# Kernel tuning notes

Hardware: AMD Instinct MI355X
Metric: run time of the kernel (lower is better)

Reference implementation:

```python
import jax, jax.numpy as jnp
import numpy as np

N, E = 50000, 800000
IN_DIM, HID, HEADS, OUT_DIM, EDGE_DIM = 128, 32, 4, 64, 32


def _glorot(key, shape, dtype=jnp.float32):
    fan_in, fan_out = shape[0], shape[1]
    lim = np.sqrt(6.0 / (fan_in + fan_out))
    return jax.random.uniform(key, shape, dtype, -lim, lim)


def setup_inputs() -> dict:
    key = jax.random.key(0)
    ks = jax.random.split(key, 16)
    H1 = HEADS * HID  # 128 = concat width of layer 1
    inp = {
        "x": jax.random.normal(ks[0], (N, IN_DIM), jnp.float32),
        "edge_index": jax.random.randint(ks[1], (2, E), 0, N, jnp.int64),
        "edge_feats": jax.random.normal(ks[2], (E, EDGE_DIM), jnp.float32),
        # layer 1: TransformerConv(128 -> 32, heads=4, concat=True, edge_dim=32)
        "Wq1": _glorot(ks[3], (IN_DIM, H1)), "bq1": jnp.zeros((H1,), jnp.float32),
        "Wk1": _glorot(ks[4], (IN_DIM, H1)), "bk1": jnp.zeros((H1,), jnp.float32),
        "Wv1": _glorot(ks[5], (IN_DIM, H1)), "bv1": jnp.zeros((H1,), jnp.float32),
        "We1": _glorot(ks[6], (EDGE_DIM, H1)),
        "Ws1": _glorot(ks[7], (IN_DIM, H1)), "bs1": jnp.zeros((H1,), jnp.float32),
        # layer 2: TransformerConv(128 -> 64, heads=1, concat=False, edge_dim=32)
        "Wq2": _glorot(ks[8], (H1, OUT_DIM)), "bq2": jnp.zeros((OUT_DIM,), jnp.float32),
        "Wk2": _glorot(ks[9], (H1, OUT_DIM)), "bk2": jnp.zeros((OUT_DIM,), jnp.float32),
        "Wv2": _glorot(ks[10], (H1, OUT_DIM)), "bv2": jnp.zeros((OUT_DIM,), jnp.float32),
        "We2": _glorot(ks[11], (EDGE_DIM, OUT_DIM)),
        "Ws2": _glorot(ks[12], (H1, OUT_DIM)), "bs2": jnp.zeros((OUT_DIM,), jnp.float32),
    }
    return inp


def _tconv(x, src, dst, e, Wq, bq, Wk, bk, Wv, bv, We, Ws, bs, heads, concat):
    """PyG TransformerConv: gather q_i/k_j/v_j, add edge embedding to k and v,
    segment-softmax over incoming edges of each target node, scatter-aggregate."""
    n = x.shape[0]
    d = Wq.shape[1] // heads
    q = (x @ Wq + bq).reshape(n, heads, d)
    k = (x @ Wk + bk).reshape(n, heads, d)
    v = (x @ Wv + bv).reshape(n, heads, d)
    ee = (e @ We).reshape(-1, heads, d)      # [E, H, D]
    kj = k[src] + ee                          # [E, H, D]
    vj = v[src] + ee                          # [E, H, D]
    a = jnp.einsum('ehd,ehd->eh', q[dst], kj) / jnp.sqrt(jnp.asarray(d, x.dtype))
    amax = jax.ops.segment_max(a, dst, num_segments=n)      # [N, H]
    ex = jnp.exp(a - amax[dst])
    den = jax.ops.segment_sum(ex, dst, num_segments=n)
    alpha = ex / den[dst]                                   # [E, H]
    out = jax.ops.segment_sum(alpha[..., None] * vj, dst, num_segments=n)
    out = out.reshape(n, heads * d) if concat else out.mean(axis=1)
    return out + x @ Ws + bs  # root/skip connection (lin_skip)


def reference(x, edge_index, edge_feats,
              Wq1, bq1, Wk1, bk1, Wv1, bv1, We1, Ws1, bs1,
              Wq2, bq2, Wk2, bk2, Wv2, bv2, We2, Ws2, bs2):
    src, dst = edge_index[0], edge_index[1]  # flow='source_to_target'
    h = _tconv(x, src, dst, edge_feats, Wq1, bq1, Wk1, bk1, Wv1, bv1,
               We1, Ws1, bs1, heads=HEADS, concat=True)
    h = jax.nn.relu(h)  # activation; dropout p=0.0 is identity
    h = _tconv(h, src, dst, edge_feats, Wq2, bq2, Wk2, bk2, Wv2, bv2,
               We2, Ws2, bs2, heads=1, concat=False)
    return h
```

## Files before the change

kernel.cpp:

```cpp
#include <hip/hip_runtime.h>
#include <hip/hip_bf16.h>


typedef unsigned int  u32;
typedef unsigned short u16;
typedef __attribute__((ext_vector_type(8))) __bf16 bf16x8;
typedef __attribute__((ext_vector_type(4))) float  f32x4;

#define S1L (0.17677669529663687f * 1.4426950408889634f)
#define S2L (0.125f * 1.4426950408889634f)

__device__ __forceinline__ u16 f2bf(float f) {
    u32 u = __float_as_uint(f);
    u32 r = (u + 0x7fffu + ((u >> 16) & 1u)) >> 16;
    return (u16)r;
}
__device__ __forceinline__ float bflo(u32 u) { return __uint_as_float(u << 16); }
__device__ __forceinline__ float bfhi(u32 u) { return __uint_as_float(u & 0xffff0000u); }

template<int CTRL>
__device__ __forceinline__ float dpp_add(float x) {
    int y = __builtin_amdgcn_mov_dpp(__float_as_int(x), CTRL, 0xF, 0xF, true);
    return x + __int_as_float(y);
}

__global__ void k_hist(const int* __restrict__ dst, int* __restrict__ deg, int nE) {
    int e = blockIdx.x * 256 + threadIdx.x;
    if (e < nE) atomicAdd(&deg[dst[e]], 1);
}

__global__ __launch_bounds__(1024) void k_scan_part(const int* __restrict__ deg,
                                                    int* __restrict__ rp,
                                                    int* __restrict__ csum, int nN)
{
    __shared__ int buf[1024];
    const int tid = threadIdx.x, idx = blockIdx.x * 1024 + tid;
    int v = (idx < nN) ? deg[idx] : 0;
    buf[tid] = v;
    __syncthreads();
    for (int off = 1; off < 1024; off <<= 1) {
        int t = (tid >= off) ? buf[tid - off] : 0;
        __syncthreads();
        buf[tid] += t;
        __syncthreads();
    }
    if (idx < nN) rp[idx] = buf[tid] - v;
    if (tid == 1023) csum[blockIdx.x] = buf[1023];
}

__global__ __launch_bounds__(1024) void k_scan_tot(int* __restrict__ csum, int nb,
                                                   int* __restrict__ rowptr, int nN, int nE)
{
    __shared__ int buf[1024];
    const int tid = threadIdx.x;
    int v = (tid < nb) ? csum[tid] : 0;
    buf[tid] = v;
    __syncthreads();
    for (int off = 1; off < 1024; off <<= 1) {
        int t = (tid >= off) ? buf[tid - off] : 0;
        __syncthreads();
        buf[tid] += t;
        __syncthreads();
    }
    if (tid < nb) csum[tid] = buf[tid] - v;
    if (tid == 0) rowptr[nN] = nE;
}

__global__ void k_scan_apply(int* __restrict__ rp, const int* __restrict__ csum,
                             int* __restrict__ fill, int nN)
{
    int i = blockIdx.x * 256 + threadIdx.x;
    if (i < nN) { int r = rp[i] + csum[i >> 10]; rp[i] = r; fill[i] = r; }
}

__global__ void k_scatter(const int* __restrict__ src, const int* __restrict__ dst,
                          const float4* __restrict__ ef4,
                          int* __restrict__ fill, int* __restrict__ srcs,
                          uint4* __restrict__ efc, int nE)
{
    int e = blockIdx.x * 256 + threadIdx.x;
    if (e < nE) {
        int p = atomicAdd(&fill[dst[e]], 1);
        srcs[p] = src[e];
        const float4* r = ef4 + (size_t)e * 8;
        uint4* w = efc + (size_t)p * 4;
        #pragma unroll
        for (int t = 0; t < 4; ++t) {
            float4 f0 = r[2 * t], f1 = r[2 * t + 1];
            w[t] = make_uint4((u32)f2bf(f0.x) | ((u32)f2bf(f0.y) << 16),
                              (u32)f2bf(f0.z) | ((u32)f2bf(f0.w) << 16),
                              (u32)f2bf(f1.x) | ((u32)f2bf(f1.y) << 16),
                              (u32)f2bf(f1.z) | ((u32)f2bf(f1.w) << 16));
        }
    }
}

__global__ void k_f2h4(const float4* __restrict__ in4, uint2* __restrict__ out4, long n4) {
    long i = (long)blockIdx.x * 256 + threadIdx.x;
    if (i < n4) {
        float4 f = in4[i];
        out4[i] = make_uint2((u32)f2bf(f.x) | ((u32)f2bf(f.y) << 16),
                             (u32)f2bf(f.z) | ((u32)f2bf(f.w) << 16));
    }
}

__global__ void k_w2t1(const float* __restrict__ Wq, const float* __restrict__ Wk,
                       const float* __restrict__ Wv, const float* __restrict__ Ws,
                       u16* __restrict__ WT)
{
    int t = blockIdx.x * 256 + threadIdx.x;
    if (t >= 512 * 128) return;
    int j = t >> 7, k = t & 127;
    int m = j >> 7, col = j & 127;
    const float* W = (m == 0) ? Wq : (m == 1) ? Wk : (m == 2) ? Wv : Ws;
    WT[t] = f2bf(W[k * 128 + col]);
}

__global__ void k_w2t2(const float* __restrict__ Wq, const float* __restrict__ Wk,
                       const float* __restrict__ Wv, const float* __restrict__ Ws,
                       u16* __restrict__ WT)
{
    int t = blockIdx.x * 256 + threadIdx.x;
    if (t >= 256 * 128) return;
    int j = t >> 7, k = t & 127;
    int m = j >> 6, col = j & 63;
    const float* W = (m == 0) ? Wq : (m == 1) ? Wk : (m == 2) ? Wv : Ws;
    WT[t] = f2bf(W[k * 64 + col]);
}

__global__ void k_wqe1(const float* __restrict__ Wq, const float* __restrict__ bq,
                       const float* __restrict__ We,
                       u16* __restrict__ WqET, float* __restrict__ bqe)
{
    int t = blockIdx.x * 256 + threadIdx.x;
    if (t >= 128 * 128) return;
    int j = t >> 7, m = t & 127;
    int h = j >> 5, c = j & 31;
    float acc = 0.f;
    #pragma unroll
    for (int d = 0; d < 32; ++d)
        acc += Wq[m * 128 + h * 32 + d] * We[c * 128 + h * 32 + d];
    WqET[j * 128 + m] = f2bf(acc * S1L);
    if (m == 0) {
        float b = 0.f;
        #pragma unroll
        for (int d = 0; d < 32; ++d)
            b += bq[h * 32 + d] * We[c * 128 + h * 32 + d];
        bqe[j] = b * S1L;
    }
}

__global__ void k_wqe2(const float* __restrict__ Wq, const float* __restrict__ bq,
                       const float* __restrict__ We,
                       u16* __restrict__ WqET, float* __restrict__ bqe)
{
    int t = blockIdx.x * 256 + threadIdx.x;
    if (t >= 32 * 128) return;
    int c = t >> 7, m = t & 127;
    float acc = 0.f;
    #pragma unroll
    for (int d = 0; d < 64; ++d)
        acc += Wq[m * 64 + d] * We[c * 64 + d];
    WqET[c * 128 + m] = f2bf(acc * S2L);
    if (m == 0) {
        float b = 0.f;
        #pragma unroll
        for (int d = 0; d < 64; ++d) b += bq[d] * We[c * 64 + d];
        bqe[c] = b * S2L;
    }
}

__global__ __launch_bounds__(256, 2) void k_lin1_mfma(
    const u16* __restrict__ xb, const u16* __restrict__ WT,
    const u16* __restrict__ WqET, const float* __restrict__ bqe,
    const float* __restrict__ bq, const float* __restrict__ bk,
    const float* __restrict__ bv, const float* __restrict__ bs,
    u32* __restrict__ qqe1, u32* __restrict__ kv1, float* __restrict__ sk1, int nN)
{
    const int wave = threadIdx.x >> 6, lane = threadIdx.x & 63;
    const int rowbase = blockIdx.x * 64 + wave * 16;
    const int colL = lane & 15;
    const int koff = (lane >> 4) * 8;
    const int arow = rowbase + colL;
    const int arow_c = arow < nN ? arow : (nN - 1);

    bf16x8 a[4];
    #pragma unroll
    for (int kk = 0; kk < 4; ++kk)
        a[kk] = *(const bf16x8*)(xb + (size_t)arow_c * 128 + kk * 32 + koff);

    u32 o_qqe[8][4]; u32 o_kv[8][4]; float o_sk[8][4];

    #pragma unroll
    for (int g = 0; g < 8; ++g) {
        const int co = g * 16 + colL;
        f32x4 aq = {0.f, 0.f, 0.f, 0.f}, ak = aq, av = aq, as_ = aq, ae = aq;
        #pragma unroll
        for (int kk = 0; kk < 4; ++kk) {
            const int kb = kk * 32 + koff;
            bf16x8 b0 = *(const bf16x8*)(WT + (size_t)(co)       * 128 + kb);
            bf16x8 b1 = *(const bf16x8*)(WT + (size_t)(128 + co) * 128 + kb);
            bf16x8 b2 = *(const bf16x8*)(WT + (size_t)(256 + co) * 128 + kb);
            bf16x8 b3 = *(const bf16x8*)(WT + (size_t)(384 + co) * 128 + kb);
            bf16x8 b4 = *(const bf16x8*)(WqET + (size_t)co * 128 + kb);
            aq  = __builtin_amdgcn_mfma_f32_16x16x32_bf16(a[kk], b0, aq,  0, 0, 0);
            ak  = __builtin_amdgcn_mfma_f32_16x16x32_bf16(a[kk], b1, ak,  0, 0, 0);
            av  = __builtin_amdgcn_mfma_f32_16x16x32_bf16(a[kk], b2, av,  0, 0, 0);
            as_ = __builtin_amdgcn_mfma_f32_16x16x32_bf16(a[kk], b3, as_, 0, 0, 0);
            ae  = __builtin_amdgcn_mfma_f32_16x16x32_bf16(a[kk], b4, ae,  0, 0, 0);
        }
        const float bqv = bq[co], bkv = bk[co], bvv = bv[co], bsv = bs[co];
        const float bev = bqe[co];
        #pragma unroll
        for (int i = 0; i < 4; ++i) {
            o_qqe[g][i] = (u32)f2bf((aq[i] + bqv) * S1L)
                        | ((u32)f2bf(ae[i] + bev) << 16);
            o_kv[g][i]  = (u32)f2bf(ak[i] + bkv) | ((u32)f2bf(av[i] + bvv) << 16);
            o_sk[g][i]  = as_[i] + bsv;
        }
    }

    const int rb = rowbase + (lane >> 4) * 4;
    #pragma unroll
    for (int i = 0; i < 4; ++i) {
        const int r = rb + i;
        if (r < nN) {
            #pragma unroll
            for (int g = 0; g < 8; ++g) {
                const int co = g * 16 + colL;
                qqe1[(size_t)r * 128 + co] = o_qqe[g][i];
                kv1 [(size_t)r * 128 + co] = o_kv[g][i];
                sk1 [(size_t)r * 128 + co] = o_sk[g][i];
            }
        }
    }
}

__global__ __launch_bounds__(256, 2) void k_lin2_mfma(
    const u16* __restrict__ hb, const u16* __restrict__ WT,
    const u16* __restrict__ WqET, const float* __restrict__ bqe,
    const float* __restrict__ bq, const float* __restrict__ bk,
    const float* __restrict__ bv, const float* __restrict__ bs,
    float* __restrict__ q2, float* __restrict__ qe2,
    u32* __restrict__ kv2, float* __restrict__ sk2, int nN)
{
    const int wave = threadIdx.x >> 6, lane = threadIdx.x & 63;
    const int rowbase = blockIdx.x * 64 + wave * 16;
    const int colL = lane & 15;
    const int koff = (lane >> 4) * 8;
    const int arow = rowbase + colL;
    const int arow_c = arow < nN ? arow : (nN - 1);

    bf16x8 a[4];
    #pragma unroll
    for (int kk = 0; kk < 4; ++kk)
        a[kk] = *(const bf16x8*)(hb + (size_t)arow_c * 128 + kk * 32 + koff);

    float o_q[4][4]; u32 o_kv[4][4]; float o_sk[4][4]; float o_qe[2][4];

    #pragma unroll
    for (int g = 0; g < 4; ++g) {
        const int co = g * 16 + colL;
        f32x4 aq = {0.f, 0.f, 0.f, 0.f}, ak = aq, av = aq, as_ = aq;
        #pragma unroll
        for (int kk = 0; kk < 4; ++kk) {
            const int kb = kk * 32 + koff;
            bf16x8 b0 = *(const bf16x8*)(WT + (size_t)(co)       * 128 + kb);
            bf16x8 b1 = *(const bf16x8*)(WT + (size_t)(64  + co) * 128 + kb);
            bf16x8 b2 = *(const bf16x8*)(WT + (size_t)(128 + co) * 128 + kb);
            bf16x8 b3 = *(const bf16x8*)(WT + (size_t)(192 + co) * 128 + kb);
            aq  = __builtin_amdgcn_mfma_f32_16x16x32_bf16(a[kk], b0, aq,  0, 0, 0);
            ak  = __builtin_amdgcn_mfma_f32_16x16x32_bf16(a[kk], b1, ak,  0, 0, 0);
            av  = __builtin_amdgcn_mfma_f32_16x16x32_bf16(a[kk], b2, av,  0, 0, 0);
            as_ = __builtin_amdgcn_mfma_f32_16x16x32_bf16(a[kk], b3, as_, 0, 0, 0);
        }
        const float bqv = bq[co], bkv = bk[co], bvv = bv[co], bsv = bs[co];
        #pragma unroll
        for (int i = 0; i < 4; ++i) {
            o_q[g][i]  = (aq[i] + bqv) * S2L;
            o_kv[g][i] = (u32)f2bf(ak[i] + bkv) | ((u32)f2bf(av[i] + bvv) << 16);
            o_sk[g][i] = as_[i] + bsv;
        }
    }
    #pragma unroll
    for (int g = 0; g < 2; ++g) {
        const int co = g * 16 + colL;
        f32x4 ae = {0.f, 0.f, 0.f, 0.f};
        #pragma unroll
        for (int kk = 0; kk < 4; ++kk) {
            const int kb = kk * 32 + koff;
            bf16x8 b4 = *(const bf16x8*)(WqET + (size_t)co * 128 + kb);
            ae = __builtin_amdgcn_mfma_f32_16x16x32_bf16(a[kk], b4, ae, 0, 0, 0);
        }
        const float bev = bqe[co];
        #pragma unroll
        for (int i = 0; i < 4; ++i) o_qe[g][i] = ae[i] + bev;
    }

    const int rb = rowbase + (lane >> 4) * 4;
    #pragma unroll
    for (int i = 0; i < 4; ++i) {
        const int r = rb + i;
        if (r < nN) {
            #pragma unroll
            for (int g = 0; g < 4; ++g) {
                const int co = g * 16 + colL;
                q2 [(size_t)r * 64 + co] = o_q[g][i];
                kv2[(size_t)r * 64 + co] = o_kv[g][i];
                sk2[(size_t)r * 64 + co] = o_sk[g][i];
            }
            #pragma unroll
            for (int g = 0; g < 2; ++g)
                qe2[(size_t)r * 32 + g * 16 + colL] = o_qe[g][i];
        }
    }
}

__global__ __launch_bounds__(256) void k_agg1(
    const int* __restrict__ rowptr, const int* __restrict__ srcs,
    const u16* __restrict__ efc, const u32* __restrict__ qqe1,
    const u32* __restrict__ kv1,
    float* __restrict__ sv1, float* __restrict__ sef1, float* __restrict__ den1, int nN)
{
    const int wave = threadIdx.x >> 6, lane = threadIdx.x & 63;
    const int d = blockIdx.x * 4 + wave;
    if (d >= nN) return;
    const int es = lane >> 5;
    const int h  = (lane >> 3) & 3;
    const int c8 = lane & 7;
    const int jb = h * 32 + c8 * 4;

    const uint4 qq = *(const uint4*)(qqe1 + (size_t)d * 128 + jb);
    const float4 qr  = {bflo(qq.x), bflo(qq.y), bflo(qq.z), bflo(qq.w)};
    const float4 qer = {bfhi(qq.x), bfhi(qq.y), bfhi(qq.z), bfhi(qq.w)};

    const int beg = rowptr[d], end = rowptr[d + 1];
    float den = 0.f;
    float4 sv = {0.f, 0.f, 0.f, 0.f}, sef = sv;

    #pragma unroll 2
    for (int i = beg; i < end; i += 2) {
        const int ie = i + es;
        const bool valid = ie < end;
        const int iec = valid ? ie : beg;
        const int s = srcs[iec];
        const uint4 kp = *(const uint4*)(kv1 + ((u32)s << 7) + jb);
        const uint2 ee = *(const uint2*)(efc + ((size_t)iec << 5) + c8 * 4);
        const float f0 = bflo(ee.x), f1 = bfhi(ee.x);
        const float f2 = bflo(ee.y), f3 = bfhi(ee.y);
        float p = qr.x * bflo(kp.x) + qr.y * bflo(kp.y)
                + qr.z * bflo(kp.z) + qr.w * bflo(kp.w)
                + qer.x * f0 + qer.y * f1 + qer.z * f2 + qer.w * f3;
        p = dpp_add<0xB1>(p);
        p = dpp_add<0x4E>(p);
        p = dpp_add<0x141>(p);
        const float ex = valid ? exp2f(p) : 0.f;
        den += ex;
        sv.x += ex * bfhi(kp.x); sv.y += ex * bfhi(kp.y);
        sv.z += ex * bfhi(kp.z); sv.w += ex * bfhi(kp.w);
        sef.x += ex * f0; sef.y += ex * f1; sef.z += ex * f2; sef.w += ex * f3;
    }
    den  += __shfl_xor(den, 32);
    sv.x += __shfl_xor(sv.x, 32); sv.y += __shfl_xor(sv.y, 32);
    sv.z += __shfl_xor(sv.z, 32); sv.w += __shfl_xor(sv.w, 32);
    sef.x += __shfl_xor(sef.x, 32); sef.y += __shfl_xor(sef.y, 32);
    sef.z += __shfl_xor(sef.z, 32); sef.w += __shfl_xor(sef.w, 32);
    if (es == 0) {
        *(float4*)(sv1  + (size_t)d * 128 + jb) = sv;
        *(float4*)(sef1 + (size_t)d * 128 + jb) = sef;
        if (c8 == 0) den1[(size_t)d * 4 + h] = den;
    }
}

__global__ __launch_bounds__(256) void k_finalize1(
    const float* __restrict__ sv1, const float* __restrict__ sef1,
    const float* __restrict__ den1, const float* __restrict__ sk1,
    const float* __restrict__ We, u16* __restrict__ h1b, int nN)
{
    const int tid = threadIdx.x;
    const int g = tid >> 7, j = tid & 127, h = j >> 5;
    float wreg[32];
    #pragma unroll
    for (int cc = 0; cc < 32; ++cc) wreg[cc] = We[cc * 128 + j];
    for (int n = blockIdx.x * 2 + g; n < nN; n += gridDim.x * 2) {
        float dd = den1[(size_t)n * 4 + h];
        float acc = sv1[(size_t)n * 128 + j];
        const float* sefp = &sef1[(size_t)n * 128 + h * 32];
        #pragma unroll
        for (int cc = 0; cc < 32; ++cc) acc = fmaf(sefp[cc], wreg[cc], acc);
        float o = (dd > 0.f ? acc / dd : 0.f) + sk1[(size_t)n * 128 + j];
        h1b[(size_t)n * 128 + j] = f2bf(o > 0.f ? o : 0.f);
    }
}

__global__ __launch_bounds__(256) void k_agg2(
    const int* __restrict__ rowptr, const int* __restrict__ srcs,
    const u16* __restrict__ efc, const float* __restrict__ q2,
    const float* __restrict__ qe2, const u32* __restrict__ kv2,
    float* __restrict__ sv2, float* __restrict__ sef2, float* __restrict__ den2, int nN)
{
    const int wave = threadIdx.x >> 6, lane = threadIdx.x & 63;
    const int d = blockIdx.x * 4 + wave;
    if (d >= nN) return;
    const int es  = lane >> 4;
    const int c16 = lane & 15;
    const int jb  = c16 * 4;
    const int ce  = (c16 & 7) * 4;

    const float4 qr = *(const float4*)(q2 + (size_t)d * 64 + jb);
    float4 qer = {0.f, 0.f, 0.f, 0.f};
    if (c16 < 8) qer = *(const float4*)(qe2 + (size_t)d * 32 + jb);

    const int beg = rowptr[d], end = rowptr[d + 1];
    float den = 0.f;
    float4 sv = {0.f, 0.f, 0.f, 0.f}, sef = sv;

    #pragma unroll 2
    for (int i = beg; i < end; i += 4) {
        const int ie = i + es;
        const bool valid = ie < end;
        const int iec = valid ? ie : beg;
        const int s = srcs[iec];
        const uint4 kp = *(const uint4*)(kv2 + ((u32)s << 6) + jb);
        const uint2 ee = *(const uint2*)(efc + ((size_t)iec << 5) + ce);
        const float f0 = bflo(ee.x), f1 = bfhi(ee.x);
        const float f2 = bflo(ee.y), f3 = bfhi(ee.y);
        float p = qr.x * bflo(kp.x) + qr.y * bflo(kp.y)
                + qr.z * bflo(kp.z) + qr.w * bflo(kp.w)
                + qer.x * f0 + qer.y * f1 + qer.z * f2 + qer.w * f3;
        p = dpp_add<0xB1>(p);
        p = dpp_add<0x4E>(p);
        p = dpp_add<0x141>(p);
        p = dpp_add<0x140>(p);
        const float ex = valid ? exp2f(p) : 0.f;
        den += ex;
        sv.x += ex * bfhi(kp.x); sv.y += ex * bfhi(kp.y);
        sv.z += ex * bfhi(kp.z); sv.w += ex * bfhi(kp.w);
        sef.x += ex * f0; sef.y += ex * f1; sef.z += ex * f2; sef.w += ex * f3;
    }
    #pragma unroll
    for (int m = 16; m <= 32; m <<= 1) {
        den  += __shfl_xor(den, m);
        sv.x += __shfl_xor(sv.x, m); sv.y += __shfl_xor(sv.y, m);
        sv.z += __shfl_xor(sv.z, m); sv.w += __shfl_xor(sv.w, m);
        sef.x += __shfl_xor(sef.x, m); sef.y += __shfl_xor(sef.y, m);
        sef.z += __shfl_xor(sef.z, m); sef.w += __shfl_xor(sef.w, m);
    }
    if (es == 0) {
        *(float4*)(sv2 + (size_t)d * 64 + jb) = sv;
        if (c16 < 8) *(float4*)(sef2 + (size_t)d * 32 + jb) = sef;
        if (c16 == 0) den2[d] = den;
    }
}

__global__ __launch_bounds__(256) void k_finalize2(
    const float* __restrict__ sv2, const float* __restrict__ sef2,
    const float* __restrict__ den2, const float* __restrict__ sk2,
    const float* __restrict__ We, float* __restrict__ out, int nN)
{
    const int tid = threadIdx.x;
    const int g = tid >> 6, c = tid & 63;
    float wreg[32];
    #pragma unroll
    for (int k = 0; k < 32; ++k) wreg[k] = We[k * 64 + c];
    for (int n = blockIdx.x * 4 + g; n < nN; n += gridDim.x * 4) {
        float dd = den2[n];
        float acc = sv2[(size_t)n * 64 + c];
        const float* sefp = &sef2[(size_t)n * 32];
        #pragma unroll
        for (int k = 0; k < 32; ++k) acc = fmaf(sefp[k], wreg[k], acc);
        out[(size_t)n * 64 + c] = (dd > 0.f ? acc / dd : 0.f) + sk2[(size_t)n * 64 + c];
    }
}

extern "C" void kernel_launch(void* const* d_in, const int* in_sizes, int n_in,
                              void* d_out, int out_size, void* d_ws, size_t ws_size,
                              hipStream_t stream)
{
    const float* x   = (const float*)d_in[0];
    const int*   ei  = (const int*)d_in[1];
    const float* ef  = (const float*)d_in[2];
    const float* Wq1 = (const float*)d_in[3];  const float* bq1 = (const float*)d_in[4];
    const float* Wk1 = (const float*)d_in[5];  const float* bk1 = (const float*)d_in[6];
    const float* Wv1 = (const float*)d_in[7];  const float* bv1 = (const float*)d_in[8];
    const float* We1 = (const float*)d_in[9];
    const float* Ws1 = (const float*)d_in[10]; const float* bs1 = (const float*)d_in[11];
    const float* Wq2 = (const float*)d_in[12]; const float* bq2 = (const float*)d_in[13];
    const float* Wk2 = (const float*)d_in[14]; const float* bk2 = (const float*)d_in[15];
    const float* Wv2 = (const float*)d_in[16]; const float* bv2 = (const float*)d_in[17];
    const float* We2 = (const float*)d_in[18];
    const float* Ws2 = (const float*)d_in[19]; const float* bs2 = (const float*)d_in[20];

    const int nN = in_sizes[0] / 128;
    const int nE = in_sizes[1] / 2;
    const int* srcv = ei;
    const int* dstv = ei + nE;

    float* ws = (float*)d_ws;
    size_t off = 0;
    auto alloc = [&](size_t n) { float* p = ws + off; off += n; return p; };
    u32*   qqe1  = (u32*)alloc((size_t)nN * 128);
    float* sk1   = alloc((size_t)nN * 128);
    u32*   kv1   = (u32*)alloc((size_t)nN * 128);
    float* sv1   = alloc((size_t)nN * 128);
    float* sef1  = alloc((size_t)nN * 128);
    u16*   h1b   = (u16*)alloc((size_t)nN * 64);
    u16*   xb    = (u16*)alloc((size_t)nN * 64);
    float* den1  = alloc((size_t)nN * 4);
    u16*   efc   = (u16*)alloc((size_t)nE * 16);
    u16*   WT1   = (u16*)alloc(512 * 128 / 2);
    u16*   WT2   = (u16*)alloc(256 * 128 / 2);
    u16*   WqET1 = (u16*)alloc(128 * 128 / 2);
    u16*   WqET2 = (u16*)alloc(32 * 128 / 2);
    float* bqe1  = alloc(128);
    float* bqe2  = alloc(32);
    int* deg     = (int*)alloc(nN);
    int* rowptr  = (int*)alloc(nN + 1);
    int* fill    = (int*)alloc(nN);
    int* csum    = (int*)alloc(1024);
    int* srcs    = (int*)alloc(nE);
    float* l2 = (float*)qqe1;
    size_t o2 = 0;
    auto alloc2 = [&](size_t n) { float* p = l2 + o2; o2 += n; return p; };
    float* q2   = alloc2((size_t)nN * 64);
    u32*   kv2  = (u32*)alloc2((size_t)nN * 64);
    float* sk2  = alloc2((size_t)nN * 64);
    float* qe2  = alloc2((size_t)nN * 32);
    float* sv2  = alloc2((size_t)nN * 64);
    float* sef2 = alloc2((size_t)nN * 32);
    float* den2 = alloc2(nN);
    (void)ws_size; (void)n_in; (void)out_size;

    const int nChunk = (nN + 1023) / 1024;
    const int gemmBlocks = (nN + 63) / 64;

    hipMemsetAsync(deg, 0, (size_t)nN * sizeof(int), stream);
    k_hist<<<(nE + 255) / 256, 256, 0, stream>>>(dstv, deg, nE);
    k_scan_part<<<nChunk, 1024, 0, stream>>>(deg, rowptr, csum, nN);
    k_scan_tot<<<1, 1024, 0, stream>>>(csum, nChunk, rowptr, nN, nE);
    k_scan_apply<<<(nN + 255) / 256, 256, 0, stream>>>(rowptr, csum, fill, nN);
    k_scatter<<<(nE + 255) / 256, 256, 0, stream>>>(
        srcv, dstv, (const float4*)ef, fill, srcs, (uint4*)efc, nE);

    k_w2t1<<<(512 * 128 + 255) / 256, 256, 0, stream>>>(Wq1, Wk1, Wv1, Ws1, WT1);
    k_w2t2<<<(256 * 128 + 255) / 256, 256, 0, stream>>>(Wq2, Wk2, Wv2, Ws2, WT2);
    k_wqe1<<<(128 * 128 + 255) / 256, 256, 0, stream>>>(Wq1, bq1, We1, WqET1, bqe1);
    k_wqe2<<<(32 * 128 + 255) / 256, 256, 0, stream>>>(Wq2, bq2, We2, WqET2, bqe2);
    long nx4 = (long)nN * 32;
    k_f2h4<<<(int)((nx4 + 255) / 256), 256, 0, stream>>>((const float4*)x, (uint2*)xb, nx4);

    k_lin1_mfma<<<gemmBlocks, 256, 0, stream>>>(
        xb, WT1, WqET1, bqe1, bq1, bk1, bv1, bs1, qqe1, kv1, sk1, nN);
    k_agg1<<<(nN + 3) / 4, 256, 0, stream>>>(
        rowptr, srcs, efc, qqe1, kv1, sv1, sef1, den1, nN);
    k_finalize1<<<1024, 256, 0, stream>>>(sv1, sef1, den1, sk1, We1, h1b, nN);

    k_lin2_mfma<<<gemmBlocks, 256, 0, stream>>>(
        h1b, WT2, WqET2, bqe2, bq2, bk2, bv2, bs2, q2, qe2, kv2, sk2, nN);
    k_agg2<<<(nN + 3) / 4, 256, 0, stream>>>(
        rowptr, srcs, efc, q2, qe2, kv2, sv2, sef2, den2, nN);
    k_finalize2<<<1024, 256, 0, stream>>>(sv2, sef2, den2, sk2, We2, (float*)d_out, nN);
}
```

Measured before the change: 432.5 us.

## Restructure node projection GEMMs as LDS-tiled 128x128 MFMA blocks over column tiles

Both projection GEMMs now stage a 128-row activation tile and a 128-column weight tile in swizzled LDS, with each wave computing a 64x64 sub-tile using 16 accumulators. The grid has a second dimension over output column groups, and all weights are packed into one concatenated buffer. Before, each wave reloaded the weight fragments straight from global memory. The change aims to raise data reuse and MFMA density, but adds LDS traffic, re-reads the activation tile once per column tile, and writes 16-bit scattered halves of the packed outputs, which may hurt write coalescing.

```diff
diff --git a/kernel.cpp b/kernel.cpp
--- a/kernel.cpp
+++ b/kernel.cpp
@@ -106,26 +106,30 @@
 
 __global__ void k_w2t1(const float* __restrict__ Wq, const float* __restrict__ Wk,
                        const float* __restrict__ Wv, const float* __restrict__ Ws,
-                       u16* __restrict__ WT)
+                       u16* __restrict__ WB)
 {
     int t = blockIdx.x * 256 + threadIdx.x;
     if (t >= 512 * 128) return;
     int j = t >> 7, k = t & 127;
     int m = j >> 7, col = j & 127;
     const float* W = (m == 0) ? Wq : (m == 1) ? Wk : (m == 2) ? Wv : Ws;
-    WT[t] = f2bf(W[k * 128 + col]);
+    WB[t] = f2bf(W[k * 128 + col]);
 }
 
 __global__ void k_w2t2(const float* __restrict__ Wq, const float* __restrict__ Wk,
                        const float* __restrict__ Wv, const float* __restrict__ Ws,
-                       u16* __restrict__ WT)
+                       u16* __restrict__ WB)
 {
     int t = blockIdx.x * 256 + threadIdx.x;
-    if (t >= 256 * 128) return;
+    if (t >= 384 * 128) return;
     int j = t >> 7, k = t & 127;
-    int m = j >> 6, col = j & 63;
-    const float* W = (m == 0) ? Wq : (m == 1) ? Wk : (m == 2) ? Wv : Ws;
-    WT[t] = f2bf(W[k * 64 + col]);
+    if (j < 256) {
+        int m = j >> 6, col = j & 63;
+        const float* W = (m == 0) ? Wq : (m == 1) ? Wk : (m == 2) ? Wv : Ws;
+        WB[t] = f2bf(W[k * 64 + col]);
+    } else if (j >= 288) {
+        WB[t] = 0;
+    }
 }
 
 __global__ void k_wqe1(const float* __restrict__ Wq, const float* __restrict__ bq,
@@ -170,148 +174,180 @@
     }
 }
 
-__global__ __launch_bounds__(256, 2) void k_lin1_mfma(
-    const u16* __restrict__ xb, const u16* __restrict__ WT,
-    const u16* __restrict__ WqET, const float* __restrict__ bqe,
+__global__ __launch_bounds__(256) void k_lin_gemm1(
+    const u16* __restrict__ xb, const u16* __restrict__ WB,
     const float* __restrict__ bq, const float* __restrict__ bk,
     const float* __restrict__ bv, const float* __restrict__ bs,
+    const float* __restrict__ bqe,
     u32* __restrict__ qqe1, u32* __restrict__ kv1, float* __restrict__ sk1, int nN)
 {
-    const int wave = threadIdx.x >> 6, lane = threadIdx.x & 63;
-    const int rowbase = blockIdx.x * 64 + wave * 16;
-    const int colL = lane & 15;
-    const int koff = (lane >> 4) * 8;
-    const int arow = rowbase + colL;
-    const int arow_c = arow < nN ? arow : (nN - 1);
-
-    bf16x8 a[4];
-    #pragma unroll
-    for (int kk = 0; kk < 4; ++kk)
-        a[kk] = *(const bf16x8*)(xb + (size_t)arow_c * 128 + kk * 32 + koff);
-
-    u32 o_qqe[8][4]; u32 o_kv[8][4]; float o_sk[8][4];
-
-    #pragma unroll
-    for (int g = 0; g < 8; ++g) {
-        const int co = g * 16 + colL;
-        f32x4 aq = {0.f, 0.f, 0.f, 0.f}, ak = aq, av = aq, as_ = aq, ae = aq;
-        #pragma unroll
-        for (int kk = 0; kk < 4; ++kk) {
-            const int kb = kk * 32 + koff;
-            bf16x8 b0 = *(const bf16x8*)(WT + (size_t)(co)       * 128 + kb);
-            bf16x8 b1 = *(const bf16x8*)(WT + (size_t)(128 + co) * 128 + kb);
-            bf16x8 b2 = *(const bf16x8*)(WT + (size_t)(256 + co) * 128 + kb);
-            bf16x8 b3 = *(const bf16x8*)(WT + (size_t)(384 + co) * 128 + kb);
-            bf16x8 b4 = *(const bf16x8*)(WqET + (size_t)co * 128 + kb);
-            aq  = __builtin_amdgcn_mfma_f32_16x16x32_bf16(a[kk], b0, aq,  0, 0, 0);
-            ak  = __builtin_amdgcn_mfma_f32_16x16x32_bf16(a[kk], b1, ak,  0, 0, 0);
-            av  = __builtin_amdgcn_mfma_f32_16x16x32_bf16(a[kk], b2, av,  0, 0, 0);
-            as_ = __builtin_amdgcn_mfma_f32_16x16x32_bf16(a[kk], b3, as_, 0, 0, 0);
-            ae  = __builtin_amdgcn_mfma_f32_16x16x32_bf16(a[kk], b4, ae,  0, 0, 0);
-        }
-        const float bqv = bq[co], bkv = bk[co], bvv = bv[co], bsv = bs[co];
-        const float bev = bqe[co];
-        #pragma unroll
-        for (int i = 0; i < 4; ++i) {
-            o_qqe[g][i] = (u32)f2bf((aq[i] + bqv) * S1L)
-                        | ((u32)f2bf(ae[i] + bev) << 16);
-            o_kv[g][i]  = (u32)f2bf(ak[i] + bkv) | ((u32)f2bf(av[i] + bvv) << 16);
-            o_sk[g][i]  = as_[i] + bsv;
-        }
-    }
-
-    const int rb = rowbase + (lane >> 4) * 4;
-    #pragma unroll
-    for (int i = 0; i < 4; ++i) {
-        const int r = rb + i;
-        if (r < nN) {
+    __shared__ __align__(16) u16 lds[2 * 128 * 128];
+    const int tid = threadIdx.x;
+    const int ct = blockIdx.y;
+    const int rowbase = blockIdx.x * 128;
+
+    {
+        const int lr = tid >> 4, kc = tid & 15;
+        #pragma unroll
+        for (int it = 0; it < 8; ++it) {
+            int row = it * 16 + lr;
+            int grow = rowbase + row; if (grow >= nN) grow = nN - 1;
+            uint4 va = *(const uint4*)(xb + (size_t)grow * 128 + kc * 8);
+            *(uint4*)((char*)lds + row * 256 + ((kc * 16) ^ ((row & 7) << 4))) = va;
+        }
+        #pragma unroll
+        for (int it = 0; it < 8; ++it) {
+            int row = it * 16 + lr;
+            uint4 vb = *(const uint4*)(WB + ((size_t)ct * 128 + row) * 128 + kc * 8);
+            *(uint4*)((char*)lds + 32768 + row * 256 + ((kc * 16) ^ ((row & 7) << 4))) = vb;
+        }
+    }
+    __syncthreads();
+
+    const int wave = tid >> 6, lane = tid & 63;
+    const int wr = wave >> 1, wc = wave & 1;
+    const int colL = lane & 15, kgrp = lane >> 4;
+
+    f32x4 acc[4][4];
+    #pragma unroll
+    for (int m = 0; m < 4; ++m)
+        #pragma unroll
+        for (int n = 0; n < 4; ++n) acc[m][n] = {0.f, 0.f, 0.f, 0.f};
+
+    #pragma unroll
+    for (int ks = 0; ks < 4; ++ks) {
+        const int kb = ks * 64 + kgrp * 16;
+        bf16x8 af[4], bfr[4];
+        #pragma unroll
+        for (int m = 0; m < 4; ++m) {
+            int row = wr * 64 + m * 16 + colL;
+            af[m] = *(const bf16x8*)((const char*)lds + row * 256 + (kb ^ ((row & 7) << 4)));
+        }
+        #pragma unroll
+        for (int n = 0; n < 4; ++n) {
+            int row = wc * 64 + n * 16 + colL;
+            bfr[n] = *(const bf16x8*)((const char*)lds + 32768 + row * 256 + (kb ^ ((row & 7) << 4)));
+        }
+        #pragma unroll
+        for (int m = 0; m < 4; ++m)
             #pragma unroll
-            for (int g = 0; g < 8; ++g) {
-                const int co = g * 16 + colL;
-                qqe1[(size_t)r * 128 + co] = o_qqe[g][i];
-                kv1 [(size_t)r * 128 + co] = o_kv[g][i];
-                sk1 [(size_t)r * 128 + co] = o_sk[g][i];
+            for (int n = 0; n < 4; ++n)
+                acc[m][n] = __builtin_amdgcn_mfma_f32_16x16x32_bf16(af[m], bfr[n], acc[m][n], 0, 0, 0);
+    }
+
+    const float* bias = (ct == 0) ? bq : (ct == 1) ? bk : (ct == 2) ? bv : (ct == 3) ? bs : bqe;
+    const float scale = (ct == 0) ? S1L : 1.f;
+    const bool  is32 = (ct == 3);
+    const int   hi = (ct == 2 || ct == 4) ? 1 : 0;
+    u32* dstw = (ct == 3) ? (u32*)sk1 : ((ct == 1 || ct == 2) ? kv1 : qqe1);
+
+    #pragma unroll
+    for (int n = 0; n < 4; ++n) {
+        const int c = wc * 64 + n * 16 + colL;
+        const float bval = bias[c];
+        #pragma unroll
+        for (int m = 0; m < 4; ++m) {
+            #pragma unroll
+            for (int i = 0; i < 4; ++i) {
+                const int r = rowbase + wr * 64 + m * 16 + kgrp * 4 + i;
+                if (r < nN) {
+                    float v = (acc[m][n][i] + bval) * scale;
+                    if (is32) ((float*)dstw)[(size_t)r * 128 + c] = v;
+                    else ((u16*)dstw)[(((size_t)r * 128 + c) << 1) + hi] = f2bf(v);
+                }
             }
         }
     }
 }
 
-__global__ __launch_bounds__(256, 2) void k_lin2_mfma(
-    const u16* __restrict__ hb, const u16* __restrict__ WT,
-    const u16* __restrict__ WqET, const float* __restrict__ bqe,
+__global__ __launch_bounds__(256) void k_lin_gemm2(
+    const u16* __restrict__ hb, const u16* __restrict__ WB,
     const float* __restrict__ bq, const float* __restrict__ bk,
     const float* __restrict__ bv, const float* __restrict__ bs,
-    float* __restrict__ q2, float* __restrict__ qe2,
-    u32* __restrict__ kv2, float* __restrict__ sk2, int nN)
-{
-    const int wave = threadIdx.x >> 6, lane = threadIdx.x & 63;
-    const int rowbase = blockIdx.x * 64 + wave * 16;
-    const int colL = lane & 15;
-    const int koff = (lane >> 4) * 8;
-    const int arow = rowbase + colL;
-    const int arow_c = arow < nN ? arow : (nN - 1);
-
-    bf16x8 a[4];
-    #pragma unroll
-    for (int kk = 0; kk < 4; ++kk)
-        a[kk] = *(const bf16x8*)(hb + (size_t)arow_c * 128 + kk * 32 + koff);
-
-    float o_q[4][4]; u32 o_kv[4][4]; float o_sk[4][4]; float o_qe[2][4];
-
-    #pragma unroll
-    for (int g = 0; g < 4; ++g) {
-        const int co = g * 16 + colL;
-        f32x4 aq = {0.f, 0.f, 0.f, 0.f}, ak = aq, av = aq, as_ = aq;
-        #pragma unroll
-        for (int kk = 0; kk < 4; ++kk) {
-            const int kb = kk * 32 + koff;
-            bf16x8 b0 = *(const bf16x8*)(WT + (size_t)(co)       * 128 + kb);
-            bf16x8 b1 = *(const bf16x8*)(WT + (size_t)(64  + co) * 128 + kb);
-            bf16x8 b2 = *(const bf16x8*)(WT + (size_t)(128 + co) * 128 + kb);
-            bf16x8 b3 = *(const bf16x8*)(WT + (size_t)(192 + co) * 128 + kb);
-            aq  = __builtin_amdgcn_mfma_f32_16x16x32_bf16(a[kk], b0, aq,  0, 0, 0);
-            ak  = __builtin_amdgcn_mfma_f32_16x16x32_bf16(a[kk], b1, ak,  0, 0, 0);
-            av  = __builtin_amdgcn_mfma_f32_16x16x32_bf16(a[kk], b2, av,  0, 0, 0);
-            as_ = __builtin_amdgcn_mfma_f32_16x16x32_bf16(a[kk], b3, as_, 0, 0, 0);
-        }
-        const float bqv = bq[co], bkv = bk[co], bvv = bv[co], bsv = bs[co];
-        #pragma unroll
-        for (int i = 0; i < 4; ++i) {
-            o_q[g][i]  = (aq[i] + bqv) * S2L;
-            o_kv[g][i] = (u32)f2bf(ak[i] + bkv) | ((u32)f2bf(av[i] + bvv) << 16);
-            o_sk[g][i] = as_[i] + bsv;
-        }
-    }
-    #pragma unroll
-    for (int g = 0; g < 2; ++g) {
-        const int co = g * 16 + colL;
-        f32x4 ae = {0.f, 0.f, 0.f, 0.f};
-        #pragma unroll
-        for (int kk = 0; kk < 4; ++kk) {
-            const int kb = kk * 32 + koff;
-            bf16x8 b4 = *(const bf16x8*)(WqET + (size_t)co * 128 + kb);
-            ae = __builtin_amdgcn_mfma_f32_16x16x32_bf16(a[kk], b4, ae, 0, 0, 0);
-        }
-        const float bev = bqe[co];
-        #pragma unroll
-        for (int i = 0; i < 4; ++i) o_qe[g][i] = ae[i] + bev;
-    }
-
-    const int rb = rowbase + (lane >> 4) * 4;
-    #pragma unroll
-    for (int i = 0; i < 4; ++i) {
-        const int r = rb + i;
-        if (r < nN) {
+    const float* __restrict__ bqe,
+    float* __restrict__ q2, u32* __restrict__ kv2, float* __restrict__ sk2,
+    float* __restrict__ qe2, int nN)
+{
+    __shared__ __align__(16) u16 lds[2 * 128 * 128];
+    const int tid = threadIdx.x;
+    const int ct = blockIdx.y;
+    const int rowbase = blockIdx.x * 128;
+
+    {
+        const int lr = tid >> 4, kc = tid & 15;
+        #pragma unroll
+        for (int it = 0; it < 8; ++it) {
+            int row = it * 16 + lr;
+            int grow = rowbase + row; if (grow >= nN) grow = nN - 1;
+            uint4 va = *(const uint4*)(hb + (size_t)grow * 128 + kc * 8);
+            *(uint4*)((char*)lds + row * 256 + ((kc * 16) ^ ((row & 7) << 4))) = va;
+        }
+        #pragma unroll
+        for (int it = 0; it < 8; ++it) {
+            int row = it * 16 + lr;
+            uint4 vb = *(const uint4*)(WB + ((size_t)ct * 128 + row) * 128 + kc * 8);
+            *(uint4*)((char*)lds + 32768 + row * 256 + ((kc * 16) ^ ((row & 7) << 4))) = vb;
+        }
+    }
+    __syncthreads();
+
+    const int wave = tid >> 6, lane = tid & 63;
+    const int wr = wave >> 1, wc = wave & 1;
+    const int colL = lane & 15, kgrp = lane >> 4;
+
+    f32x4 acc[4][4];
+    #pragma unroll
+    for (int m = 0; m < 4; ++m)
+        #pragma unroll
+        for (int n = 0; n < 4; ++n) acc[m][n] = {0.f, 0.f, 0.f, 0.f};
+
+    #pragma unroll
+    for (int ks = 0; ks < 4; ++ks) {
+        const int kb = ks * 64 + kgrp * 16;
+        bf16x8 af[4], bfr[4];
+        #pragma unroll
+        for (int m = 0; m < 4; ++m) {
+            int row = wr * 64 + m * 16 + colL;
+            af[m] = *(const bf16x8*)((const char*)lds + row * 256 + (kb ^ ((row & 7) << 4)));
+        }
+        #pragma unroll
+        for (int n = 0; n < 4; ++n) {
+            int row = wc * 64 + n * 16 + colL;
+            bfr[n] = *(const bf16x8*)((const char*)lds + 32768 + row * 256 + (kb ^ ((row & 7) << 4)));
+        }
+        #pragma unroll
+        for (int m = 0; m < 4; ++m)
             #pragma unroll
-            for (int g = 0; g < 4; ++g) {
-                const int co = g * 16 + colL;
-                q2 [(size_t)r * 64 + co] = o_q[g][i];
-                kv2[(size_t)r * 64 + co] = o_kv[g][i];
-                sk2[(size_t)r * 64 + co] = o_sk[g][i];
+            for (int n = 0; n < 4; ++n)
+                acc[m][n] = __builtin_amdgcn_mfma_f32_16x16x32_bf16(af[m], bfr[n], acc[m][n], 0, 0, 0);
+    }
+
+    const int mode = ct * 2 + wc;
+    if (mode == 5) return;
+
+    #pragma unroll
+    for (int n = 0; n < 4; ++n) {
+        const int cl = n * 16 + colL;
+        float bval;
+        if (mode == 0) bval = bq[cl];
+        else if (mode == 1) bval = bk[cl];
+        else if (mode == 2) bval = bv[cl];
+        else if (mode == 3) bval = bs[cl];
+        else bval = (cl < 32) ? bqe[cl] : 0.f;
+        #pragma unroll
+        for (int m = 0; m < 4; ++m) {
+            #pragma unroll
+            for (int i = 0; i < 4; ++i) {
+                const int r = rowbase + wr * 64 + m * 16 + kgrp * 4 + i;
+                if (r < nN) {
+                    const float v = acc[m][n][i] + bval;
+                    if (mode == 0)      q2[(size_t)r * 64 + cl] = v * S2L;
+                    else if (mode == 1) ((u16*)kv2)[(((size_t)r * 64 + cl) << 1)] = f2bf(v);
+                    else if (mode == 2) ((u16*)kv2)[(((size_t)r * 64 + cl) << 1) + 1] = f2bf(v);
+                    else if (mode == 3) sk2[(size_t)r * 64 + cl] = v;
+                    else if (cl < 32)   qe2[(size_t)r * 32 + cl] = v;
+                }
             }
-            #pragma unroll
-            for (int g = 0; g < 2; ++g)
-                qe2[(size_t)r * 32 + g * 16 + colL] = o_qe[g][i];
         }
     }
 }
@@ -508,10 +544,8 @@
     u16*   xb    = (u16*)alloc((size_t)nN * 64);
     float* den1  = alloc((size_t)nN * 4);
     u16*   efc   = (u16*)alloc((size_t)nE * 16);
-    u16*   WT1   = (u16*)alloc(512 * 128 / 2);
-    u16*   WT2   = (u16*)alloc(256 * 128 / 2);
-    u16*   WqET1 = (u16*)alloc(128 * 128 / 2);
-    u16*   WqET2 = (u16*)alloc(32 * 128 / 2);
+    u16*   WB1   = (u16*)alloc(640 * 128 / 2);
+    u16*   WB2   = (u16*)alloc(384 * 128 / 2);
     float* bqe1  = alloc(128);
     float* bqe2  = alloc(32);
     int* deg     = (int*)alloc(nN);
@@ -532,7 +566,7 @@
     (void)ws_size; (void)n_in; (void)out_size;
 
     const int nChunk = (nN + 1023) / 1024;
-    const int gemmBlocks = (nN + 63) / 64;
+    const int rowTiles = (nN + 127) / 128;
 
     hipMemsetAsync(deg, 0, (size_t)nN * sizeof(int), stream);
     k_hist<<<(nE + 255) / 256, 256, 0, stream>>>(dstv, deg, nE);
@@ -542,21 +576,21 @@
     k_scatter<<<(nE + 255) / 256, 256, 0, stream>>>(
         srcv, dstv, (const float4*)ef, fill, srcs, (uint4*)efc, nE);
 
-    k_w2t1<<<(512 * 128 + 255) / 256, 256, 0, stream>>>(Wq1, Wk1, Wv1, Ws1, WT1);
-    k_w2t2<<<(256 * 128 + 255) / 256, 256, 0, stream>>>(Wq2, Wk2, Wv2, Ws2, WT2);
-    k_wqe1<<<(128 * 128 + 255) / 256, 256, 0, stream>>>(Wq1, bq1, We1, WqET1, bqe1);
-    k_wqe2<<<(32 * 128 + 255) / 256, 256, 0, stream>>>(Wq2, bq2, We2, WqET2, bqe2);
+    k_w2t1<<<(512 * 128 + 255) / 256, 256, 0, stream>>>(Wq1, Wk1, Wv1, Ws1, WB1);
+    k_w2t2<<<(384 * 128 + 255) / 256, 256, 0, stream>>>(Wq2, Wk2, Wv2, Ws2, WB2);
+    k_wqe1<<<(128 * 128 + 255) / 256, 256, 0, stream>>>(Wq1, bq1, We1, WB1 + 512 * 128, bqe1);
+    k_wqe2<<<(32 * 128 + 255) / 256, 256, 0, stream>>>(Wq2, bq2, We2, WB2 + 256 * 128, bqe2);
     long nx4 = (long)nN * 32;
     k_f2h4<<<(int)((nx4 + 255) / 256), 256, 0, stream>>>((const float4*)x, (uint2*)xb, nx4);
 
-    k_lin1_mfma<<<gemmBlocks, 256, 0, stream>>>(
-        xb, WT1, WqET1, bqe1, bq1, bk1, bv1, bs1, qqe1, kv1, sk1, nN);
+    k_lin_gemm1<<<dim3(rowTiles, 5), 256, 0, stream>>>(
+        xb, WB1, bq1, bk1, bv1, bs1, bqe1, qqe1, kv1, sk1, nN);
     k_agg1<<<(nN + 3) / 4, 256, 0, stream>>>(
         rowptr, srcs, efc, qqe1, kv1, sv1, sef1, den1, nN);
     k_finalize1<<<1024, 256, 0, stream>>>(sv1, sef1, den1, sk1, We1, h1b, nN);
 
-    k_lin2_mfma<<<gemmBlocks, 256, 0, stream>>>(
-        h1b, WT2, WqET2, bqe2, bq2, bk2, bv2, bs2, q2, qe2, kv2, sk2, nN);
+    k_lin_gemm2<<<dim3(rowTiles, 3), 256, 0, stream>>>(
+        h1b, WB2, bq2, bk2, bv2, bs2, bqe2, q2, kv2, sk2, qe2, nN);
     k_agg2<<<(nN + 3) / 4, 256, 0, stream>>>(
         rowptr, srcs, efc, q2, qe2, kv2, sv2, sef2, den2, nN);
     k_finalize2<<<1024, 256, 0, stream>>>(sv2, sef2, den2, sk2, We2, (float*)d_out, nN);
```

After: 417.1 us. -3.6%, faster.
